# Performance work log

Measured on AMD Instinct MI355X. Metric: run time of the kernel, lower is better.

The kernel has to match this reference:

```python
import jax, jax.numpy as jnp
import numpy as np

B, T, E, D, A, V, EMB = 256, 64, 2048, 512, 512, 10000, 256

def _glorot(key, shape):
    lim = np.sqrt(6.0 / (shape[0] + shape[-1]))
    return jax.random.uniform(key, shape, jnp.float32, -lim, lim)

def setup_inputs() -> dict:
    key = jax.random.key(0)
    ks = jax.random.split(key, 16)
    return {
        'input_c': jax.random.randint(ks[0], (B, 1), 0, V),
        'hidden': jax.random.normal(ks[1], (B, D), jnp.float32),
        'carry': jax.random.normal(ks[2], (B, D), jnp.float32),
        'encoder_output': jax.random.normal(ks[3], (B, T, E), jnp.float32),
        'emb': jax.random.normal(ks[4], (V, EMB), jnp.float32) * 0.05,
        'w1': _glorot(ks[5], (D, A)),  'b1': jnp.zeros((A,), jnp.float32),
        'w2': _glorot(ks[6], (E, A)),  'b2': jnp.zeros((A,), jnp.float32),
        'v':  _glorot(ks[7], (A, 1)),  'bv': jnp.zeros((1,), jnp.float32),
        'wx': _glorot(ks[8], (E + EMB, 4 * D)),
        'wh': _glorot(ks[9], (D, 4 * D)),
        'bl': jnp.zeros((4 * D,), jnp.float32),
        'wp': _glorot(ks[10], (D, V)), 'bp': jnp.zeros((V,), jnp.float32),
    }

def reference(input_c, hidden, carry, encoder_output, emb, w1, b1, w2, b2, v, bv, wx, wh, bl, wp, bp):
    # embedding: [B,1] -> [B,EMB] after squeeze
    x = emb[input_c[:, 0]]
    # Bahdanau additive attention: score = v^T tanh(W1 h + W2 enc)
    q = hidden @ w1 + b1                                # [B,A]
    k = jnp.einsum('bte,ea->bta', encoder_output, w2) + b2  # [B,T,A]
    score = jnp.tanh(q[:, None, :] + k) @ v + bv        # [B,T,1]
    attn = jax.nn.softmax(score, axis=1)                # [B,T,1]
    context = jnp.sum(attn * encoder_output, axis=1)    # [B,E]
    # LSTM cell (keras gate order i,f,c,o); dropout inactive (training=False)
    lstm_in = jnp.concatenate([context, x], axis=-1)    # [B,E+EMB]
    z = lstm_in @ wx + hidden @ wh + bl                 # [B,4D]
    i, f, g, o = jnp.split(z, 4, axis=-1)
    c_new = jax.nn.sigmoid(f) * carry + jax.nn.sigmoid(i) * jnp.tanh(g)
    h_new = jax.nn.sigmoid(o) * jnp.tanh(c_new)
    logits = h_new @ wp + bp                            # [B,V]
    return logits, h_new, c_new
```

## Files before the change

kernel.cpp:

```cpp
#include <hip/hip_runtime.h>
#include <hip/hip_bf16.h>
#include <math.h>

#define BB 256
#define TT 64
#define EE 2048
#define DD 512
#define AA 512
#define VV 10000
#define VPAD 10240
#define EMBD 256
#define KLSTM (EE + EMBD + DD)
#define N4D (4 * DD)
#define MROWS (BB * TT)

using bf16x8 = __attribute__((ext_vector_type(8))) __bf16;
using f32x4  = __attribute__((ext_vector_type(4))) float;

__device__ __forceinline__ float sigf(float x) { return 1.f / (1.f + expf(-x)); }

__global__ void k_q(const float* __restrict__ hidden, const float* __restrict__ w1,
                    const float* __restrict__ b1, const float* __restrict__ b2,
                    float* __restrict__ qq) {
    __shared__ float hs[DD];
    const int b = blockIdx.x, tid = threadIdx.x;
    {
        float2 hv = *(const float2*)&hidden[(size_t)b * DD + 2 * tid];
        hs[2 * tid] = hv.x; hs[2 * tid + 1] = hv.y;
    }
    __syncthreads();
    const int a0 = 2 * tid;
    float2 acc = {0.f, 0.f};
    #pragma unroll 4
    for (int k = 0; k < DD; ++k) {
        float2 w = *(const float2*)&w1[(size_t)k * AA + a0];
        float h = hs[k];
        acc.x = fmaf(h, w.x, acc.x);
        acc.y = fmaf(h, w.y, acc.y);
    }
    qq[(size_t)b * AA + a0]     = acc.x + b1[a0]     + b2[a0];
    qq[(size_t)b * AA + a0 + 1] = acc.y + b1[a0 + 1] + b2[a0 + 1];
}

__global__ void k_w2t(const float* __restrict__ w2, __bf16* __restrict__ w2t) {
    __shared__ float t[32][33];
    const int k0 = blockIdx.x * 32, n0 = blockIdx.y * 32;
    const int tx = threadIdx.x, ty = threadIdx.y;
    #pragma unroll
    for (int i = 0; i < 4; ++i)
        t[ty + 8 * i][tx] = w2[(size_t)(k0 + ty + 8 * i) * AA + n0 + tx];
    __syncthreads();
    #pragma unroll
    for (int i = 0; i < 4; ++i)
        w2t[(size_t)(n0 + ty + 8 * i) * EE + k0 + tx] = (__bf16)t[tx][ty + 8 * i];
}

__global__ void k_wxht(const float* __restrict__ wx, const float* __restrict__ wh,
                       __bf16* __restrict__ wt) {
    __shared__ float t[32][33];
    const int k0 = blockIdx.x * 32, n0 = blockIdx.y * 32;
    const int tx = threadIdx.x, ty = threadIdx.y;
    #pragma unroll
    for (int i = 0; i < 4; ++i) {
        int k = k0 + ty + 8 * i;
        const float* wrow = (k < EE + EMBD) ? &wx[(size_t)k * N4D] : &wh[(size_t)(k - EE - EMBD) * N4D];
        t[ty + 8 * i][tx] = wrow[n0 + tx];
    }
    __syncthreads();
    #pragma unroll
    for (int i = 0; i < 4; ++i)
        wt[(size_t)(n0 + ty + 8 * i) * KLSTM + k0 + tx] = (__bf16)t[tx][ty + 8 * i];
}

__global__ void k_wpt(const float* __restrict__ wp, __bf16* __restrict__ wpt) {
    __shared__ float t[32][33];
    const int k0 = blockIdx.x * 32, n0 = blockIdx.y * 32;
    const int tx = threadIdx.x, ty = threadIdx.y;
    #pragma unroll
    for (int i = 0; i < 4; ++i) {
        int n = n0 + tx;
        t[ty + 8 * i][tx] = wp[(size_t)(k0 + ty + 8 * i) * VV + (n < VV ? n : VV - 1)];
    }
    __syncthreads();
    #pragma unroll
    for (int i = 0; i < 4; ++i)
        wpt[(size_t)(n0 + ty + 8 * i) * DD + k0 + tx] = (__bf16)t[tx][ty + 8 * i];
}

__global__ __launch_bounds__(256, 4) void k_score(
        const float* __restrict__ enc, const __bf16* __restrict__ w2t,
        const float* __restrict__ qq, const float* __restrict__ vvec,
        float* __restrict__ spart) {
    __shared__ bf16x8 Abuf[64][8];
    __shared__ bf16x8 Bbuf[128][8];
    __shared__ float qsv[128], vsv[128], wredL[2][64];
    const int tid = threadIdx.x;
    const int mb = blockIdx.x & 255, nb = blockIdx.x >> 8;
    const int m0 = mb * 64, n0 = nb * 128;
    const int l = tid & 63, wv = tid >> 6;
    const int wm = wv >> 1, wn = wv & 1;
    const int ar = l & 15, agr = l >> 4;

    if (tid < 128) qsv[tid] = qq[(size_t)mb * AA + n0 + tid];
    else           vsv[tid - 128] = vvec[n0 + tid - 128];

    const int arow = tid >> 2, ag0 = (tid & 3) * 2;
    const float* aptr = enc + (size_t)(m0 + arow) * EE + ag0 * 8;
    const int brow = tid >> 1, bg0 = (tid & 1) * 4;
    const __bf16* bptr = w2t + (size_t)(n0 + brow) * EE + bg0 * 8;

    f32x4 acc[2][4];
    #pragma unroll
    for (int mi = 0; mi < 2; ++mi)
        #pragma unroll
        for (int ni = 0; ni < 4; ++ni)
            acc[mi][ni] = (f32x4){0.f, 0.f, 0.f, 0.f};

    float4 af[4];
    bf16x8 bstg[4];
    #pragma unroll
    for (int j = 0; j < 4; ++j) af[j] = *(const float4*)(aptr + j * 4);
    #pragma unroll
    for (int i = 0; i < 4; ++i) bstg[i] = *(const bf16x8*)(bptr + i * 8);

    const int NIT = EE / 64;
    for (int it = 0; it < NIT; ++it) {
        if (it > 0) __syncthreads();
        {
            bf16x8 pk;
            pk[0] = (__bf16)af[0].x; pk[1] = (__bf16)af[0].y; pk[2] = (__bf16)af[0].z; pk[3] = (__bf16)af[0].w;
            pk[4] = (__bf16)af[1].x; pk[5] = (__bf16)af[1].y; pk[6] = (__bf16)af[1].z; pk[7] = (__bf16)af[1].w;
            Abuf[arow][ag0 ^ (arow & 7)] = pk;
            pk[0] = (__bf16)af[2].x; pk[1] = (__bf16)af[2].y; pk[2] = (__bf16)af[2].z; pk[3] = (__bf16)af[2].w;
            pk[4] = (__bf16)af[3].x; pk[5] = (__bf16)af[3].y; pk[6] = (__bf16)af[3].z; pk[7] = (__bf16)af[3].w;
            Abuf[arow][(ag0 + 1) ^ (arow & 7)] = pk;
        }
        #pragma unroll
        for (int i = 0; i < 4; ++i)
            Bbuf[brow][(bg0 + i) ^ (brow & 7)] = bstg[i];
        if (it + 1 < NIT) {
            const int k1 = (it + 1) * 64;
            #pragma unroll
            for (int j = 0; j < 4; ++j) af[j] = *(const float4*)(aptr + k1 + j * 4);
            #pragma unroll
            for (int i = 0; i < 4; ++i) bstg[i] = *(const bf16x8*)(bptr + k1 + i * 8);
        }
        __syncthreads();
        #pragma unroll
        for (int ks = 0; ks < 2; ++ks) {
            bf16x8 afr[2], bfr[4];
            #pragma unroll
            for (int mi = 0; mi < 2; ++mi)
                afr[mi] = Abuf[wm * 32 + mi * 16 + ar][(ks * 4 + agr) ^ (ar & 7)];
            #pragma unroll
            for (int ni = 0; ni < 4; ++ni)
                bfr[ni] = Bbuf[wn * 64 + ni * 16 + ar][(ks * 4 + agr) ^ (ar & 7)];
            #pragma unroll
            for (int mi = 0; mi < 2; ++mi)
                #pragma unroll
                for (int ni = 0; ni < 4; ++ni)
                    acc[mi][ni] = __builtin_amdgcn_mfma_f32_16x16x32_bf16(afr[mi], bfr[ni], acc[mi][ni], 0, 0, 0);
        }
    }

    float sred[2][4];
    #pragma unroll
    for (int mi = 0; mi < 2; ++mi)
        #pragma unroll
        for (int r = 0; r < 4; ++r) sred[mi][r] = 0.f;
    #pragma unroll
    for (int ni = 0; ni < 4; ++ni) {
        const int col = wn * 64 + ni * 16 + ar;
        const float qa = qsv[col], va = vsv[col];
        #pragma unroll
        for (int mi = 0; mi < 2; ++mi)
            #pragma unroll
            for (int r = 0; r < 4; ++r)
                sred[mi][r] += tanhf(qa + acc[mi][ni][r]) * va;
    }
    #pragma unroll
    for (int mi = 0; mi < 2; ++mi)
        #pragma unroll
        for (int r = 0; r < 4; ++r) {
            #pragma unroll
            for (int off = 1; off < 16; off <<= 1)
                sred[mi][r] += __shfl_xor(sred[mi][r], off, 64);
        }
    if (ar == 0) {
        #pragma unroll
        for (int mi = 0; mi < 2; ++mi)
            #pragma unroll
            for (int r = 0; r < 4; ++r)
                wredL[wn][wm * 32 + mi * 16 + agr * 4 + r] = sred[mi][r];
    }
    __syncthreads();
    if (tid < 64)
        spart[(size_t)nb * MROWS + m0 + tid] = wredL[0][tid] + wredL[1][tid];
}

__global__ void k_context(const float* __restrict__ enc, const float* __restrict__ spart,
                          const float* __restrict__ bv, float* __restrict__ ctx) {
    __shared__ float attn[TT];
    const int b = blockIdx.y;
    const int tid = threadIdx.x;
    if (tid < 64) {
        const int m = b * TT + tid;
        float s = spart[m] + spart[MROWS + m] + spart[2 * MROWS + m] + spart[3 * MROWS + m] + bv[0];
        float mx = s;
        #pragma unroll
        for (int off = 1; off < 64; off <<= 1) mx = fmaxf(mx, __shfl_xor(mx, off, 64));
        float p = expf(s - mx);
        float sum = p;
        #pragma unroll
        for (int off = 1; off < 64; off <<= 1) sum += __shfl_xor(sum, off, 64);
        attn[tid] = p / sum;
    }
    __syncthreads();
    const int e = blockIdx.x * 1024 + tid * 4;
    const float* encb = enc + (size_t)b * TT * EE + e;
    float4 acc = {0.f, 0.f, 0.f, 0.f};
    #pragma unroll 4
    for (int t = 0; t < TT; ++t) {
        float a = attn[t];
        float4 ev = *(const float4*)&encb[(size_t)t * EE];
        acc.x = fmaf(a, ev.x, acc.x);
        acc.y = fmaf(a, ev.y, acc.y);
        acc.z = fmaf(a, ev.z, acc.z);
        acc.w = fmaf(a, ev.w, acc.w);
    }
    *(float4*)&ctx[(size_t)b * EE + e] = acc;
}

#define ZKS 4
#define ZKC (KLSTM / ZKS)
#define ZNIT (ZKC / 32)
__global__ void k_z(const float* __restrict__ ctx, const float* __restrict__ emb,
                    const int* __restrict__ cidx, const float* __restrict__ hidden,
                    const __bf16* __restrict__ wt, float* __restrict__ zp) {
    __shared__ bf16x8 Abuf[32][ZKC / 8];
    __shared__ int cbs[32];
    const int tid = threadIdx.x;
    const int l = tid & 63, wv = tid >> 6;
    const int b0  = blockIdx.y * 32;
    const int kc0 = blockIdx.z * ZKC;
    const int nw  = blockIdx.x * 256 + wv * 64;

    if (tid < 32) cbs[tid] = cidx[b0 + tid];
    __syncthreads();

    {
        const int srow = tid >> 3, g0 = tid & 7;
        const int bg = b0 + srow;
        const int erow = cbs[srow];
        #pragma unroll
        for (int i = 0; i < 11; ++i) {
            int g = g0 + 8 * i;
            int k = kc0 + g * 8;
            const float* src;
            if (k < EE)             src = &ctx[(size_t)bg * EE + k];
            else if (k < EE + EMBD) src = &emb[(size_t)erow * EMBD + (k - EE)];
            else                    src = &hidden[(size_t)bg * DD + (k - EE - EMBD)];
            float4 u0 = *(const float4*)src;
            float4 u1 = *(const float4*)(src + 4);
            bf16x8 pk;
            pk[0] = (__bf16)u0.x; pk[1] = (__bf16)u0.y; pk[2] = (__bf16)u0.z; pk[3] = (__bf16)u0.w;
            pk[4] = (__bf16)u1.x; pk[5] = (__bf16)u1.y; pk[6] = (__bf16)u1.z; pk[7] = (__bf16)u1.w;
            Abuf[srow][g ^ (srow & 7)] = pk;
        }
    }
    __syncthreads();

    const int ar = l & 15, agr = l >> 4;
    const __bf16* bbase = wt + (size_t)(nw + ar) * KLSTM + kc0 + agr * 8;

    f32x4 acc[2][4];
    #pragma unroll
    for (int mt = 0; mt < 2; ++mt)
        #pragma unroll
        for (int f = 0; f < 4; ++f)
            acc[mt][f] = (f32x4){0.f, 0.f, 0.f, 0.f};

    bf16x8 bA[4], bBv[4];
    #pragma unroll
    for (int f = 0; f < 4; ++f)
        bA[f] = *(const bf16x8*)(bbase + (size_t)f * 16 * KLSTM);

    for (int itp = 0; itp < ZNIT / 2; ++itp) {
        const int it0 = 2 * itp, it1 = 2 * itp + 1;
        #pragma unroll
        for (int f = 0; f < 4; ++f)
            bBv[f] = *(const bf16x8*)(bbase + (size_t)f * 16 * KLSTM + it1 * 32);
        {
            bf16x8 a0 = Abuf[ar][(it0 * 4 + agr) ^ (ar & 7)];
            bf16x8 a1 = Abuf[16 + ar][(it0 * 4 + agr) ^ (ar & 7)];
            #pragma unroll
            for (int f = 0; f < 4; ++f) {
                acc[0][f] = __builtin_amdgcn_mfma_f32_16x16x32_bf16(a0, bA[f], acc[0][f], 0, 0, 0);
                acc[1][f] = __builtin_amdgcn_mfma_f32_16x16x32_bf16(a1, bA[f], acc[1][f], 0, 0, 0);
            }
        }
        const int it2 = (it1 + 1 < ZNIT) ? it1 + 1 : it1;
        #pragma unroll
        for (int f = 0; f < 4; ++f)
            bA[f] = *(const bf16x8*)(bbase + (size_t)f * 16 * KLSTM + it2 * 32);
        {
            bf16x8 a0 = Abuf[ar][(it1 * 4 + agr) ^ (ar & 7)];
            bf16x8 a1 = Abuf[16 + ar][(it1 * 4 + agr) ^ (ar & 7)];
            #pragma unroll
            for (int f = 0; f < 4; ++f) {
                acc[0][f] = __builtin_amdgcn_mfma_f32_16x16x32_bf16(a0, bBv[f], acc[0][f], 0, 0, 0);
                acc[1][f] = __builtin_amdgcn_mfma_f32_16x16x32_bf16(a1, bBv[f], acc[1][f], 0, 0, 0);
            }
        }
    }

    float* zpo = zp + (size_t)blockIdx.z * BB * N4D;
    #pragma unroll
    for (int mt = 0; mt < 2; ++mt)
        #pragma unroll
        for (int f = 0; f < 4; ++f)
            #pragma unroll
            for (int r = 0; r < 4; ++r)
                zpo[(size_t)(b0 + mt * 16 + agr * 4 + r) * N4D + nw + f * 16 + ar] = acc[mt][f][r];
}

__global__ void k_gates(const float* __restrict__ zp, const float* __restrict__ carry,
                        const float* __restrict__ bl,
                        float* __restrict__ hout, float* __restrict__ cout) {
    const int b = blockIdx.x, tid = threadIdx.x;
    const size_t P = (size_t)BB * N4D;
    #pragma unroll
    for (int r = 0; r < 2; ++r) {
        int d = tid + r * 256;
        float zi = bl[d], zf = bl[DD + d], zg = bl[2 * DD + d], zo = bl[3 * DD + d];
        #pragma unroll
        for (int ks = 0; ks < ZKS; ++ks) {
            const float* zb = zp + ks * P + (size_t)b * N4D;
            zi += zb[d];
            zf += zb[DD + d];
            zg += zb[2 * DD + d];
            zo += zb[3 * DD + d];
        }
        float c = carry[(size_t)b * DD + d];
        float cn = sigf(zf) * c + sigf(zi) * tanhf(zg);
        float hn = sigf(zo) * tanhf(cn);
        cout[(size_t)b * DD + d] = cn;
        hout[(size_t)b * DD + d] = hn;
    }
}

__global__ __launch_bounds__(256, 4) void k_logits(
        const float* __restrict__ hnew, const __bf16* __restrict__ wpt,
        const float* __restrict__ bp, float* __restrict__ logits) {
    __shared__ bf16x8 Abuf[64][8];
    __shared__ bf16x8 Bbuf[128][8];
    __shared__ float bps[128];
    const int tid = threadIdx.x;
    const int nb = blockIdx.x % 80, mb = blockIdx.x / 80;
    const int m0 = mb * 64, n0 = nb * 128;
    const int l = tid & 63, wv = tid >> 6;
    const int wm = wv >> 1, wn = wv & 1;
    const int ar = l & 15, agr = l >> 4;

    if (tid < 128) {
        int j = n0 + tid;
        bps[tid] = (j < VV) ? bp[j] : 0.f;
    }

    const int arow = tid >> 2, ag0 = (tid & 3) * 2;
    const float* aptr = hnew + (size_t)(m0 + arow) * DD + ag0 * 8;
    const int brow = tid >> 1, bg0 = (tid & 1) * 4;
    const __bf16* bptr = wpt + (size_t)(n0 + brow) * DD + bg0 * 8;

    f32x4 acc[2][4];
    #pragma unroll
    for (int mi = 0; mi < 2; ++mi)
        #pragma unroll
        for (int ni = 0; ni < 4; ++ni)
            acc[mi][ni] = (f32x4){0.f, 0.f, 0.f, 0.f};

    float4 af[4];
    bf16x8 bstg[4];
    #pragma unroll
    for (int j = 0; j < 4; ++j) af[j] = *(const float4*)(aptr + j * 4);
    #pragma unroll
    for (int i = 0; i < 4; ++i) bstg[i] = *(const bf16x8*)(bptr + i * 8);

    const int NIT = DD / 64;
    for (int it = 0; it < NIT; ++it) {
        if (it > 0) __syncthreads();
        {
            bf16x8 pk;
            pk[0] = (__bf16)af[0].x; pk[1] = (__bf16)af[0].y; pk[2] = (__bf16)af[0].z; pk[3] = (__bf16)af[0].w;
            pk[4] = (__bf16)af[1].x; pk[5] = (__bf16)af[1].y; pk[6] = (__bf16)af[1].z; pk[7] = (__bf16)af[1].w;
            Abuf[arow][ag0 ^ (arow & 7)] = pk;
            pk[0] = (__bf16)af[2].x; pk[1] = (__bf16)af[2].y; pk[2] = (__bf16)af[2].z; pk[3] = (__bf16)af[2].w;
            pk[4] = (__bf16)af[3].x; pk[5] = (__bf16)af[3].y; pk[6] = (__bf16)af[3].z; pk[7] = (__bf16)af[3].w;
            Abuf[arow][(ag0 + 1) ^ (arow & 7)] = pk;
        }
        #pragma unroll
        for (int i = 0; i < 4; ++i)
            Bbuf[brow][(bg0 + i) ^ (brow & 7)] = bstg[i];
        if (it + 1 < NIT) {
            const int k1 = (it + 1) * 64;
            #pragma unroll
            for (int j = 0; j < 4; ++j) af[j] = *(const float4*)(aptr + k1 + j * 4);
            #pragma unroll
            for (int i = 0; i < 4; ++i) bstg[i] = *(const bf16x8*)(bptr + k1 + i * 8);
        }
        __syncthreads();
        #pragma unroll
        for (int ks = 0; ks < 2; ++ks) {
            bf16x8 afr[2], bfr[4];
            #pragma unroll
            for (int mi = 0; mi < 2; ++mi)
                afr[mi] = Abuf[wm * 32 + mi * 16 + ar][(ks * 4 + agr) ^ (ar & 7)];
            #pragma unroll
            for (int ni = 0; ni < 4; ++ni)
                bfr[ni] = Bbuf[wn * 64 + ni * 16 + ar][(ks * 4 + agr) ^ (ar & 7)];
            #pragma unroll
            for (int mi = 0; mi < 2; ++mi)
                #pragma unroll
                for (int ni = 0; ni < 4; ++ni)
                    acc[mi][ni] = __builtin_amdgcn_mfma_f32_16x16x32_bf16(afr[mi], bfr[ni], acc[mi][ni], 0, 0, 0);
        }
    }

    #pragma unroll
    for (int mi = 0; mi < 2; ++mi)
        #pragma unroll
        for (int ni = 0; ni < 4; ++ni) {
            const int colL = wn * 64 + ni * 16 + ar;
            const int col = n0 + colL;
            if (col < VV) {
                const float bb = bps[colL];
                #pragma unroll
                for (int r = 0; r < 4; ++r) {
                    const int row = m0 + wm * 32 + mi * 16 + agr * 4 + r;
                    logits[(size_t)row * VV + col] = acc[mi][ni][r] + bb;
                }
            }
        }
}

extern "C" void kernel_launch(void* const* d_in, const int* in_sizes, int n_in,
                              void* d_out, int out_size, void* d_ws, size_t ws_size,
                              hipStream_t stream) {
    const int*   cidx   = (const int*)d_in[0];
    const float* hidden = (const float*)d_in[1];
    const float* carry  = (const float*)d_in[2];
    const float* enc    = (const float*)d_in[3];
    const float* emb    = (const float*)d_in[4];
    const float* w1     = (const float*)d_in[5];
    const float* b1     = (const float*)d_in[6];
    const float* w2     = (const float*)d_in[7];
    const float* b2     = (const float*)d_in[8];
    const float* vvec   = (const float*)d_in[9];
    const float* bv     = (const float*)d_in[10];
    const float* wx     = (const float*)d_in[11];
    const float* wh     = (const float*)d_in[12];
    const float* bl     = (const float*)d_in[13];
    const float* wp     = (const float*)d_in[14];
    const float* bp     = (const float*)d_in[15];

    float* out    = (float*)d_out;
    float* logits = out;
    float* hout   = out + (size_t)BB * VV;
    float* cout   = hout + (size_t)BB * DD;

    float* ws    = (float*)d_ws;
    float* qq    = ws;
    float* score = qq + (size_t)BB * AA;
    float* ctx   = score + (size_t)BB * TT;
    float* zp    = ctx + (size_t)BB * EE;
    __bf16* wxh_t = (__bf16*)(zp + (size_t)ZKS * BB * N4D);
    float* spart = (float*)(wxh_t + (size_t)N4D * KLSTM);
    __bf16* wpt  = (__bf16*)(spart + (size_t)4 * MROWS);
    __bf16* w2t  = (__bf16*)ctx;

    hipLaunchKernelGGL(k_w2t,     dim3(EE / 32, AA / 32),    dim3(32, 8), 0, stream, w2, w2t);
    hipLaunchKernelGGL(k_wxht,    dim3(KLSTM / 32, N4D / 32), dim3(32, 8), 0, stream, wx, wh, wxh_t);
    hipLaunchKernelGGL(k_wpt,     dim3(DD / 32, VPAD / 32),  dim3(32, 8), 0, stream, wp, wpt);
    hipLaunchKernelGGL(k_q,       dim3(BB),                  dim3(256), 0, stream, hidden, w1, b1, b2, qq);
    hipLaunchKernelGGL(k_score,   dim3(1024),                dim3(256), 0, stream, enc, w2t, qq, vvec, spart);
    hipLaunchKernelGGL(k_context, dim3(2, BB),               dim3(256), 0, stream, enc, spart, bv, ctx);
    hipLaunchKernelGGL(k_z,       dim3(N4D / 256, BB / 32, ZKS), dim3(256), 0, stream, ctx, emb, cidx, hidden, wxh_t, zp);
    hipLaunchKernelGGL(k_gates,   dim3(BB),                  dim3(256), 0, stream, zp, carry, bl, hout, cout);
    hipLaunchKernelGGL(k_logits,  dim3(320),                 dim3(256), 0, stream, hout, wpt, bp, logits);
}
```

Before: 208.1 us.

## Fuse attention score and softmax into one per-batch kernel covering all A columns

The score kernel now runs one 512-thread block per batch row that covers all 512 attention columns, so each encoder tile is read and converted to bf16 only once instead of once per column block. The softmax moves into this kernel, removing the partial-score buffer and the cross-block reduction in the context kernel. B fragments are read straight from global memory (w2t, likely cache-resident) rather than staged in LDS, and the encoder tile is double-buffered with a single barrier per iteration. The cost is 256 large blocks at one block per SM with 64 accumulators per thread, which lowers occupancy and latency hiding.

```diff
diff --git a/kernel.cpp b/kernel.cpp
--- a/kernel.cpp
+++ b/kernel.cpp
@@ -87,99 +87,95 @@
         wpt[(size_t)(n0 + ty + 8 * i) * DD + k0 + tx] = (__bf16)t[tx][ty + 8 * i];
 }
 
-__global__ __launch_bounds__(256, 4) void k_score(
+__global__ __launch_bounds__(512, 1) void k_attn(
         const float* __restrict__ enc, const __bf16* __restrict__ w2t,
         const float* __restrict__ qq, const float* __restrict__ vvec,
-        float* __restrict__ spart) {
-    __shared__ bf16x8 Abuf[64][8];
-    __shared__ bf16x8 Bbuf[128][8];
-    __shared__ float qsv[128], vsv[128], wredL[2][64];
+        const float* __restrict__ bv, float* __restrict__ attnG) {
+    __shared__ bf16x8 Abuf[2][64][8];
+    __shared__ float qs[AA], vs[AA];
+    __shared__ float wred[8][64];
+    const int b = blockIdx.x;
     const int tid = threadIdx.x;
-    const int mb = blockIdx.x & 255, nb = blockIdx.x >> 8;
-    const int m0 = mb * 64, n0 = nb * 128;
     const int l = tid & 63, wv = tid >> 6;
-    const int wm = wv >> 1, wn = wv & 1;
+    const int n0w = wv * 64;
     const int ar = l & 15, agr = l >> 4;
 
-    if (tid < 128) qsv[tid] = qq[(size_t)mb * AA + n0 + tid];
-    else           vsv[tid - 128] = vvec[n0 + tid - 128];
-
-    const int arow = tid >> 2, ag0 = (tid & 3) * 2;
-    const float* aptr = enc + (size_t)(m0 + arow) * EE + ag0 * 8;
-    const int brow = tid >> 1, bg0 = (tid & 1) * 4;
-    const __bf16* bptr = w2t + (size_t)(n0 + brow) * EE + bg0 * 8;
-
-    f32x4 acc[2][4];
-    #pragma unroll
-    for (int mi = 0; mi < 2; ++mi)
+    qs[tid] = qq[(size_t)b * AA + tid];
+    vs[tid] = vvec[tid];
+
+    const int srow = tid >> 3, skseg = tid & 7;
+    const float* encrow = enc + ((size_t)b * TT + srow) * EE + skseg * 8;
+    const int sg = skseg ^ (srow & 7);
+
+    const __bf16* bbase = w2t + (size_t)(n0w + ar) * EE + agr * 8;
+
+    f32x4 acc[4][4];
+    #pragma unroll
+    for (int mi = 0; mi < 4; ++mi)
         #pragma unroll
         for (int ni = 0; ni < 4; ++ni)
             acc[mi][ni] = (f32x4){0.f, 0.f, 0.f, 0.f};
 
-    float4 af[4];
-    bf16x8 bstg[4];
-    #pragma unroll
-    for (int j = 0; j < 4; ++j) af[j] = *(const float4*)(aptr + j * 4);
-    #pragma unroll
-    for (int i = 0; i < 4; ++i) bstg[i] = *(const bf16x8*)(bptr + i * 8);
+    {
+        float4 u0 = *(const float4*)(encrow);
+        float4 u1 = *(const float4*)(encrow + 4);
+        bf16x8 pk;
+        pk[0] = (__bf16)u0.x; pk[1] = (__bf16)u0.y; pk[2] = (__bf16)u0.z; pk[3] = (__bf16)u0.w;
+        pk[4] = (__bf16)u1.x; pk[5] = (__bf16)u1.y; pk[6] = (__bf16)u1.z; pk[7] = (__bf16)u1.w;
+        Abuf[0][srow][sg] = pk;
+    }
+    __syncthreads();
 
     const int NIT = EE / 64;
     for (int it = 0; it < NIT; ++it) {
-        if (it > 0) __syncthreads();
-        {
-            bf16x8 pk;
-            pk[0] = (__bf16)af[0].x; pk[1] = (__bf16)af[0].y; pk[2] = (__bf16)af[0].z; pk[3] = (__bf16)af[0].w;
-            pk[4] = (__bf16)af[1].x; pk[5] = (__bf16)af[1].y; pk[6] = (__bf16)af[1].z; pk[7] = (__bf16)af[1].w;
-            Abuf[arow][ag0 ^ (arow & 7)] = pk;
-            pk[0] = (__bf16)af[2].x; pk[1] = (__bf16)af[2].y; pk[2] = (__bf16)af[2].z; pk[3] = (__bf16)af[2].w;
-            pk[4] = (__bf16)af[3].x; pk[5] = (__bf16)af[3].y; pk[6] = (__bf16)af[3].z; pk[7] = (__bf16)af[3].w;
-            Abuf[arow][(ag0 + 1) ^ (arow & 7)] = pk;
-        }
-        #pragma unroll
-        for (int i = 0; i < 4; ++i)
-            Bbuf[brow][(bg0 + i) ^ (brow & 7)] = bstg[i];
-        if (it + 1 < NIT) {
-            const int k1 = (it + 1) * 64;
-            #pragma unroll
-            for (int j = 0; j < 4; ++j) af[j] = *(const float4*)(aptr + k1 + j * 4);
-            #pragma unroll
-            for (int i = 0; i < 4; ++i) bstg[i] = *(const bf16x8*)(bptr + k1 + i * 8);
-        }
-        __syncthreads();
+        const int cur = it & 1;
+        float4 p0, p1;
+        const bool more = (it + 1 < NIT);
+        if (more) {
+            p0 = *(const float4*)(encrow + (it + 1) * 64);
+            p1 = *(const float4*)(encrow + (it + 1) * 64 + 4);
+        }
         #pragma unroll
         for (int ks = 0; ks < 2; ++ks) {
-            bf16x8 afr[2], bfr[4];
-            #pragma unroll
-            for (int mi = 0; mi < 2; ++mi)
-                afr[mi] = Abuf[wm * 32 + mi * 16 + ar][(ks * 4 + agr) ^ (ar & 7)];
+            bf16x8 bfr[4], afr[4];
             #pragma unroll
             for (int ni = 0; ni < 4; ++ni)
-                bfr[ni] = Bbuf[wn * 64 + ni * 16 + ar][(ks * 4 + agr) ^ (ar & 7)];
-            #pragma unroll
-            for (int mi = 0; mi < 2; ++mi)
+                bfr[ni] = *(const bf16x8*)(bbase + (size_t)(ni * 16) * EE + it * 64 + ks * 32);
+            #pragma unroll
+            for (int mi = 0; mi < 4; ++mi)
+                afr[mi] = Abuf[cur][mi * 16 + ar][(ks * 4 + agr) ^ (ar & 7)];
+            #pragma unroll
+            for (int mi = 0; mi < 4; ++mi)
                 #pragma unroll
                 for (int ni = 0; ni < 4; ++ni)
                     acc[mi][ni] = __builtin_amdgcn_mfma_f32_16x16x32_bf16(afr[mi], bfr[ni], acc[mi][ni], 0, 0, 0);
         }
-    }
-
-    float sred[2][4];
-    #pragma unroll
-    for (int mi = 0; mi < 2; ++mi)
+        if (more) {
+            bf16x8 pk;
+            pk[0] = (__bf16)p0.x; pk[1] = (__bf16)p0.y; pk[2] = (__bf16)p0.z; pk[3] = (__bf16)p0.w;
+            pk[4] = (__bf16)p1.x; pk[5] = (__bf16)p1.y; pk[6] = (__bf16)p1.z; pk[7] = (__bf16)p1.w;
+            Abuf[cur ^ 1][srow][sg] = pk;
+        }
+        __syncthreads();
+    }
+
+    float sred[4][4];
+    #pragma unroll
+    for (int mi = 0; mi < 4; ++mi)
         #pragma unroll
         for (int r = 0; r < 4; ++r) sred[mi][r] = 0.f;
     #pragma unroll
     for (int ni = 0; ni < 4; ++ni) {
-        const int col = wn * 64 + ni * 16 + ar;
-        const float qa = qsv[col], va = vsv[col];
-        #pragma unroll
-        for (int mi = 0; mi < 2; ++mi)
+        const int col = n0w + ni * 16 + ar;
+        const float qa = qs[col], va = vs[col];
+        #pragma unroll
+        for (int mi = 0; mi < 4; ++mi)
             #pragma unroll
             for (int r = 0; r < 4; ++r)
                 sred[mi][r] += tanhf(qa + acc[mi][ni][r]) * va;
     }
     #pragma unroll
-    for (int mi = 0; mi < 2; ++mi)
+    for (int mi = 0; mi < 4; ++mi)
         #pragma unroll
         for (int r = 0; r < 4; ++r) {
             #pragma unroll
@@ -188,33 +184,33 @@
         }
     if (ar == 0) {
         #pragma unroll
-        for (int mi = 0; mi < 2; ++mi)
+        for (int mi = 0; mi < 4; ++mi)
             #pragma unroll
             for (int r = 0; r < 4; ++r)
-                wredL[wn][wm * 32 + mi * 16 + agr * 4 + r] = sred[mi][r];
-    }
-    __syncthreads();
-    if (tid < 64)
-        spart[(size_t)nb * MROWS + m0 + tid] = wredL[0][tid] + wredL[1][tid];
-}
-
-__global__ void k_context(const float* __restrict__ enc, const float* __restrict__ spart,
-                          const float* __restrict__ bv, float* __restrict__ ctx) {
+                wred[wv][mi * 16 + agr * 4 + r] = sred[mi][r];
+    }
+    __syncthreads();
+    if (tid < 64) {
+        float s = bv[0];
+        #pragma unroll
+        for (int w = 0; w < 8; ++w) s += wred[w][tid];
+        float mx = s;
+        #pragma unroll
+        for (int off = 1; off < 64; off <<= 1) mx = fmaxf(mx, __shfl_xor(mx, off, 64));
+        float p = expf(s - mx);
+        float sum = p;
+        #pragma unroll
+        for (int off = 1; off < 64; off <<= 1) sum += __shfl_xor(sum, off, 64);
+        attnG[(size_t)b * TT + tid] = p / sum;
+    }
+}
+
+__global__ void k_context(const float* __restrict__ enc, const float* __restrict__ attnG,
+                          float* __restrict__ ctx) {
     __shared__ float attn[TT];
     const int b = blockIdx.y;
     const int tid = threadIdx.x;
-    if (tid < 64) {
-        const int m = b * TT + tid;
-        float s = spart[m] + spart[MROWS + m] + spart[2 * MROWS + m] + spart[3 * MROWS + m] + bv[0];
-        float mx = s;
-        #pragma unroll
-        for (int off = 1; off < 64; off <<= 1) mx = fmaxf(mx, __shfl_xor(mx, off, 64));
-        float p = expf(s - mx);
-        float sum = p;
-        #pragma unroll
-        for (int off = 1; off < 64; off <<= 1) sum += __shfl_xor(sum, off, 64);
-        attn[tid] = p / sum;
-    }
+    if (tid < 64) attn[tid] = attnG[(size_t)b * TT + tid];
     __syncthreads();
     const int e = blockIdx.x * 1024 + tid * 4;
     const float* encb = enc + (size_t)b * TT * EE + e;
@@ -470,20 +466,19 @@
 
     float* ws    = (float*)d_ws;
     float* qq    = ws;
-    float* score = qq + (size_t)BB * AA;
-    float* ctx   = score + (size_t)BB * TT;
+    float* attnG = qq + (size_t)BB * AA;
+    float* ctx   = attnG + (size_t)BB * TT;
     float* zp    = ctx + (size_t)BB * EE;
     __bf16* wxh_t = (__bf16*)(zp + (size_t)ZKS * BB * N4D);
-    float* spart = (float*)(wxh_t + (size_t)N4D * KLSTM);
-    __bf16* wpt  = (__bf16*)(spart + (size_t)4 * MROWS);
+    __bf16* wpt  = (__bf16*)(wxh_t + (size_t)N4D * KLSTM);
     __bf16* w2t  = (__bf16*)ctx;
 
     hipLaunchKernelGGL(k_w2t,     dim3(EE / 32, AA / 32),    dim3(32, 8), 0, stream, w2, w2t);
     hipLaunchKernelGGL(k_wxht,    dim3(KLSTM / 32, N4D / 32), dim3(32, 8), 0, stream, wx, wh, wxh_t);
     hipLaunchKernelGGL(k_wpt,     dim3(DD / 32, VPAD / 32),  dim3(32, 8), 0, stream, wp, wpt);
     hipLaunchKernelGGL(k_q,       dim3(BB),                  dim3(256), 0, stream, hidden, w1, b1, b2, qq);
-    hipLaunchKernelGGL(k_score,   dim3(1024),                dim3(256), 0, stream, enc, w2t, qq, vvec, spart);
-    hipLaunchKernelGGL(k_context, dim3(2, BB),               dim3(256), 0, stream, enc, spart, bv, ctx);
+    hipLaunchKernelGGL(k_attn,    dim3(BB),                  dim3(512), 0, stream, enc, w2t, qq, vvec, bv, attnG);
+    hipLaunchKernelGGL(k_context, dim3(2, BB),               dim3(256), 0, stream, enc, attnG, ctx);
     hipLaunchKernelGGL(k_z,       dim3(N4D / 256, BB / 32, ZKS), dim3(256), 0, stream, ctx, emb, cidx, hidden, wxh_t, zp);
     hipLaunchKernelGGL(k_gates,   dim3(BB),                  dim3(256), 0, stream, zp, carry, bl, hout, cout);
     hipLaunchKernelGGL(k_logits,  dim3(320),                 dim3(256), 0, stream, hout, wpt, bp, logits);
```

After: 207.5 us. Within noise of the previous version (-0.3%).
